# Performance work log

Measured on AMD Instinct MI355X. Metric: run time of the kernel, lower is better.

Reference implementation:

```python
import jax, jax.numpy as jnp
import numpy as np

R_FACTOR = 5  # reduction factor r from Tacotron.__init__


def _gru(x, h, Wx, Wh, b):
    # standard GRU cell: z,r,candidate gates packed along last dim of Wx/Wh/b
    H = h.shape[-1]
    gx = x @ Wx
    gh = h @ Wh
    z = jax.nn.sigmoid(gx[..., :H] + gh[..., :H] + b[:H])
    r = jax.nn.sigmoid(gx[..., H:2 * H] + gh[..., H:2 * H] + b[H:2 * H])
    c = jnp.tanh(gx[..., 2 * H:] + r * gh[..., 2 * H:] + b[2 * H:])
    return (1.0 - z) * h + z * c


def setup_inputs() -> dict:
    key = jax.random.key(0)
    ks = jax.random.split(key, 16)
    T_out, B, D = 1000, 128, 80     # decoder frames, batch, mel dim
    T_in, H, P = 512, 256, 128      # encoder steps, hidden, prenet out
    n = lambda k, shp, d: jax.random.normal(k, shp, dtype=jnp.float32) * (1.0 / np.sqrt(d))
    return {
        "outputs": jax.random.normal(ks[0], (T_out, B, D), dtype=jnp.float32),
        "memory": jax.random.normal(ks[1], (T_in, B, H), dtype=jnp.float32),
        "W_pre0": n(ks[2], (D, H), D), "b_pre0": jnp.zeros((H,), jnp.float32),
        "W_pre1": n(ks[3], (H, P), H), "b_pre1": jnp.zeros((P,), jnp.float32),
        "Wx_att": n(ks[4], (P, 3 * H), P), "Wh_att": n(ks[5], (H, 3 * H), H), "b_att": jnp.zeros((3 * H,), jnp.float32),
        "Wq": n(ks[6], (H, H), H), "Wm": n(ks[7], (H, H), H), "v_att": n(ks[8], (H,), H),
        "Wx_d0": n(ks[9], (2 * H, 3 * H), 2 * H), "Wh_d0": n(ks[10], (H, 3 * H), H), "b_d0": jnp.zeros((3 * H,), jnp.float32),
        "Wx_d1": n(ks[11], (H, 3 * H), H), "Wh_d1": n(ks[12], (H, 3 * H), H), "b_d1": jnp.zeros((3 * H,), jnp.float32),
        "Wo": n(ks[13], (H, D), H), "bo": jnp.zeros((D,), jnp.float32),
    }


def _forward(outputs, memory, W_pre0, b_pre0, W_pre1, b_pre1, Wx_att, Wh_att, b_att,
             Wq, Wm, v_att, Wx_d0, Wh_d0, b_d0, Wx_d1, Wh_d1, b_d1, Wo, bo):
    r = R_FACTOR
    T_out, B, D = outputs.shape
    H = memory.shape[-1]
    R = T_out // r  # reduced_time_steps
    # teacher-forcing frame per reduced step: indic[t*r + r - 1] with r zero-frames
    # prepended == outputs[t*r - 1] for t>=1, zeros for t=0.
    frames = jnp.concatenate(
        [jnp.zeros((1, B, D), outputs.dtype), outputs[r - 1::r][: R - 1]], axis=0)  # [R,B,D]
    # precompute attention keys once (AttModule over static memory)
    keys = jnp.einsum('tbh,hk->tbk', memory, Wm)  # [T_in,B,H]
    h0 = jnp.zeros((B, H), outputs.dtype)

    def step(state, frame):
        h_att, h_d0, h_d1 = state
        # pre-net (dropout inactive: inference-mode reference)
        pre = jax.nn.relu(frame @ W_pre0 + b_pre0)
        pre = jax.nn.relu(pre @ W_pre1 + b_pre1)
        # attention RNN
        query = _gru(pre, h_att, Wx_att, Wh_att, b_att)  # [B,H]
        # additive attention
        e = jnp.einsum('tbk,k->tb', jnp.tanh(keys + query @ Wq), v_att)  # [T_in,B]
        alpha = jax.nn.softmax(e, axis=0)
        context = jnp.einsum('tb,tbh->bh', alpha, memory)  # [B,H]
        # decoder cell 0 conditioned on context, with residual from query
        out0 = _gru(jnp.concatenate([query, context], axis=-1), h_d0, Wx_d0, Wh_d0, b_d0)
        res0 = query + out0
        # residual-wrapped decoder cell 1
        out1 = _gru(res0, h_d1, Wx_d1, Wh_d1, b_d1)
        res1 = res0 + out1
        dense = res1 @ Wo + bo  # [B,D]
        return (query, out0, out1), (dense, alpha)

    _, (dense_seq, alpha_seq) = jax.lax.scan(step, (h0, h0, h0), frames)
    # each reduced-step output is written to r consecutive output frames
    final_output = jnp.repeat(dense_seq, r, axis=0)  # [T_out,B,D]
    return final_output, alpha_seq  # alpha_seq: [R,B,T_in]... axes (R,T_in,B) -> transpose


def reference(outputs, memory, W_pre0, b_pre0, W_pre1, b_pre1, Wx_att, Wh_att, b_att,
              Wq, Wm, v_att, Wx_d0, Wh_d0, b_d0, Wx_d1, Wh_d1, b_d1, Wo, bo):
    final_output, alpha_seq = _forward(outputs, memory, W_pre0, b_pre0, W_pre1, b_pre1,
                                       Wx_att, Wh_att, b_att, Wq, Wm, v_att,
                                       Wx_d0, Wh_d0, b_d0, Wx_d1, Wh_d1, b_d1, Wo, bo)
    # alpha stacked per reduced step, shape [R, T_in, B] -> [R, B, T_in] as in TF reshape
    final_alpha = jnp.transpose(alpha_seq, (0, 2, 1))
    return final_output, final_alpha
```

## Files before the change

### kernel.cpp

```cpp
#include <hip/hip_runtime.h>

namespace {
constexpr int B = 128;
constexpr int D = 80;
constexpr int H = 256;
constexpr int PP = 128;
constexpr int TIN = 512;
constexpr int RSTEPS = 200;
constexpr int RF = 5;
constexpr int HB = H * B;
}

__device__ __forceinline__ float sigm(float x) { return 1.f / (1.f + __expf(-x)); }
__device__ __forceinline__ float tanh_(float x) { return 1.f - 2.f / (__expf(2.f * x) + 1.f); }
__device__ __forceinline__ unsigned short f2bf(float f) {
  unsigned int u = __float_as_uint(f);
  u += 0x7fffu + ((u >> 16) & 1u);
  return (unsigned short)(u >> 16);
}
__device__ __forceinline__ void bf2x(unsigned int w, float& f0, float& f1) {
  f0 = __uint_as_float(w << 16);
  f1 = __uint_as_float(w & 0xffff0000u);
}
__device__ __forceinline__ void unpack8(uint4 w, float* f) {
  bf2x(w.x, f[0], f[1]); bf2x(w.y, f[2], f[3]);
  bf2x(w.z, f[4], f[5]); bf2x(w.w, f[6], f[7]);
}
__device__ __forceinline__ float dot8(uint4 w, float4 x0, float4 x1) {
  float f0, f1, a;
  bf2x(w.x, f0, f1); a  = f0 * x0.x + f1 * x0.y;
  bf2x(w.y, f0, f1); a += f0 * x0.z + f1 * x0.w;
  bf2x(w.z, f0, f1); a += f0 * x1.x + f1 * x1.y;
  bf2x(w.w, f0, f1); a += f0 * x1.z + f1 * x1.w;
  return a;
}

__global__ __launch_bounds__(256) void k_keys(const float* __restrict__ mem,
                                              const float* __restrict__ Wm,
                                              unsigned short* __restrict__ keysB,
                                              unsigned short* __restrict__ memB) {
  const int k = threadIdx.x;
  const int bb = blockIdx.x >> 4, t0 = (blockIdx.x & 15) * 32;
  const float* base = mem + (size_t)t0 * (B * H) + (size_t)bb * H;
  float acc[32];
#pragma unroll
  for (int i = 0; i < 32; ++i) acc[i] = 0.f;
  for (int h = 0; h < H; h += 4) {
    const float w0 = Wm[(h + 0) * H + k];
    const float w1 = Wm[(h + 1) * H + k];
    const float w2 = Wm[(h + 2) * H + k];
    const float w3 = Wm[(h + 3) * H + k];
#pragma unroll
    for (int ti = 0; ti < 32; ++ti) {
      const float4 x = *reinterpret_cast<const float4*>(base + (size_t)ti * (B * H) + h);
      acc[ti] += x.x * w0 + x.y * w1 + x.z * w2 + x.w * w3;
    }
  }
#pragma unroll
  for (int ti = 0; ti < 32; ++ti) {
    const size_t o = ((size_t)bb * TIN + t0 + ti) * H + k;
    keysB[o] = f2bf(acc[ti]);
    memB[o] = f2bf(base[(size_t)ti * (B * H) + k]);
  }
}

__global__ __launch_bounds__(256) void k_packWq(const float* __restrict__ W,
                                                unsigned short* __restrict__ Wp) {
  const int idx = blockIdx.x * 256 + threadIdx.x;
  const int k = idx >> 8, c = idx & 255;
  Wp[(((size_t)(k >> 3) * 256) + c) * 8 + (k & 7)] = f2bf(W[idx]);
}

__global__ __launch_bounds__(256) void k_packG(const float* __restrict__ W,
                                               unsigned short* __restrict__ dst,
                                               int K, int rowOff) {
  const int idx = blockIdx.x * 256 + threadIdx.x;
  if (idx >= K * 768) return;
  const int k = idx / 768, c = idx - k * 768;
  const int g = c >> 8, j = c & 255;
  dst[((size_t)(rowOff + k) * 128 + (j >> 1)) * 8 + (j & 1) * 4 + g] = f2bf(W[idx]);
}

__global__ __launch_bounds__(256) void k_prenet(
    const float* __restrict__ outs, const float* __restrict__ Wp0,
    const float* __restrict__ bp0, const float* __restrict__ Wp1,
    const float* __restrict__ bp1, float* __restrict__ preT) {
  const int t = blockIdx.x >> 7, b = blockIdx.x & 127, tid = threadIdx.x;
  __shared__ float f[80];
  __shared__ float p0[256];
  __shared__ float s2[256];
  if (tid < 80)
    f[tid] = (t == 0) ? 0.f
                      : __builtin_nontemporal_load(
                            &outs[((size_t)(t * RF - 1) * B + b) * D + tid]);
  __syncthreads();
  {
    float a = bp0[tid];
#pragma unroll 8
    for (int k = 0; k < 80; ++k) a += f[k] * Wp0[k * 256 + tid];
    p0[tid] = fmaxf(a, 0.f);
  }
  __syncthreads();
  {
    const int c = tid & 127, kh = tid >> 7;
    float a = 0.f;
#pragma unroll 8
    for (int k = kh * 128; k < kh * 128 + 128; ++k) a += p0[k] * Wp1[k * 128 + c];
    s2[kh * 128 + c] = a;
  }
  __syncthreads();
  if (tid < 128)
    preT[((size_t)t * PP + tid) * B + b] = fmaxf(bp1[tid] + s2[tid] + s2[128 + tid], 0.f);
}

template <int NJP>
__device__ void gru_body(const unsigned short* __restrict__ wp, int K1, int K2,
                         int KH, const float* __restrict__ xT1,
                         const float* __restrict__ xT2,
                         const float* __restrict__ pctx0,
                         const float* __restrict__ msp,
                         const float* __restrict__ hT_old,
                         const float* __restrict__ b3, float* __restrict__ hT_new,
                         const float* __restrict__ resInT,
                         float* __restrict__ resOutT, int rel, float* smem) {
  const int tid = threadIdx.x;
  float* part = smem;
  float* red = smem + 8 * NJP * 512;
  const int grp = rel >> 1, bh = rel & 1;
  const int lane = tid & 63, wv = tid >> 6;
  const int b = bh * 64 + lane;

  float c0 = 0.f, c1 = 0.f;
  if (pctx0) {
    const float m0 = msp[b], s0 = msp[B + b];
    const float m1 = msp[2 * B + b], s1 = msp[3 * B + b];
    const float M = fmaxf(m0, m1);
    const float e0 = __expf(m0 - M), e1 = __expf(m1 - M);
    const float inv = 1.f / (s0 * e0 + s1 * e1);
    c0 = e0 * inv; c1 = e1 * inv;
  }

  const uint4* wp4 = reinterpret_cast<const uint4*>(wp);
  const int K12 = K1 + K2, KT = K12 + KH;
  const int KS = KT >> 3;
  const int k0 = wv * KS, k1 = k0 + KS;

  float acc[NJP * 8];
#pragma unroll
  for (int i = 0; i < NJP * 8; ++i) acc[i] = 0.f;
  float f0, f1;

#define UPD(wq, xv, base, CS)                                                  \
  bf2x(wq.x, f0, f1); acc[base + 0] += f0 * xv; acc[base + 1] += f1 * xv;      \
  bf2x(wq.y, f0, f1); acc[base + CS] += f0 * xv;                               \
  bf2x(wq.z, f0, f1); acc[base + 4] += f0 * xv; acc[base + 5] += f1 * xv;      \
  bf2x(wq.w, f0, f1); acc[base + 4 + CS] += f0 * xv;

  const int e1i = (k1 < K1) ? k1 : K1;
#pragma unroll 2
  for (int k = k0; k < e1i; ++k) {
    const float x = xT1[k * B + b];
#pragma unroll
    for (int p = 0; p < NJP; ++p) {
      const uint4 w = wp4[(size_t)k * 128 + grp * NJP + p];
      UPD(w, x, p * 8, 2)
    }
  }
  const int s2i = (k0 > K1) ? k0 : K1, e2i = (k1 < K12) ? k1 : K12;
#pragma unroll 2
  for (int k = s2i; k < e2i; ++k) {
    const int kk = k - K1;
    const float x = pctx0 ? (c0 * pctx0[kk * B + b] + c1 * pctx0[(256 + kk) * B + b])
                          : xT2[kk * B + b];
#pragma unroll
    for (int p = 0; p < NJP; ++p) {
      const uint4 w = wp4[(size_t)k * 128 + grp * NJP + p];
      UPD(w, x, p * 8, 2)
    }
  }
  const int s3i = (k0 > K12) ? k0 : K12;
#pragma unroll 2
  for (int k = s3i; k < k1; ++k) {
    const float x = hT_old[(k - K12) * B + b];
#pragma unroll
    for (int p = 0; p < NJP; ++p) {
      const uint4 w = wp4[(size_t)k * 128 + grp * NJP + p];
      UPD(w, x, p * 8, 3)
    }
  }
#undef UPD

  float* pw = part + wv * (NJP * 512);
#pragma unroll
  for (int i = 0; i < NJP * 8; ++i) pw[i * 64 + lane] = acc[i];
  __syncthreads();
  for (int idx = tid; idx < NJP * 512; idx += 512) {
    float s = 0.f;
#pragma unroll
    for (int w = 0; w < 8; ++w) s += part[w * (NJP * 512) + idx];
    red[idx] = s;
  }
  __syncthreads();
  if (tid < NJP * 128) {
    const int jl = tid >> 6, ln = tid & 63;
    const int j = grp * (NJP * 2) + jl;
    const int bb = bh * 64 + ln;
    const float az = red[(jl * 4 + 0) * 64 + ln];
    const float ar = red[(jl * 4 + 1) * 64 + ln];
    const float acx = red[(jl * 4 + 2) * 64 + ln];
    const float ach = red[(jl * 4 + 3) * 64 + ln];
    const float z = sigm(az + b3[j]);
    const float r = sigm(ar + b3[H + j]);
    const float c = tanh_(acx + r * ach + b3[2 * H + j]);
    const float hold = hT_old[j * B + bb];
    const float hn = (1.f - z) * hold + z * c;
    hT_new[j * B + bb] = hn;
    if (resOutT) resOutT[j * B + bb] = resInT[j * B + bb] + hn;
  }
}

__device__ void dense_body(int s, int b, const float* __restrict__ res1T,
                           const float* __restrict__ Wo,
                           const float* __restrict__ bo, float* __restrict__ dout,
                           const float* __restrict__ pvalsS,
                           const float* __restrict__ msS,
                           float* __restrict__ alpha, float* smem) {
  const int tid = threadIdx.x;
  float* red = smem;
  float* part = smem + 256;
  if (tid < 256) red[tid] = res1T[tid * B + b];
  __syncthreads();
  {
    const int ks = tid >> 7, c = tid & 127;
    float a = 0.f;
    if (c < D) {
#pragma unroll 8
      for (int k = ks * 64; k < ks * 64 + 64; ++k) a += red[k] * Wo[k * D + c];
    }
    part[ks * 128 + c] = a;
  }
  __syncthreads();
  if (tid < D) {
    float dv = bo[tid];
#pragma unroll
    for (int ks = 0; ks < 4; ++ks) dv += part[ks * 128 + tid];
    const size_t base = (size_t)s * RF * (B * D) + (size_t)b * D + tid;
#pragma unroll
    for (int i = 0; i < RF; ++i)
      __builtin_nontemporal_store(dv, &dout[base + (size_t)i * (B * D)]);
  }
  const float m0 = msS[b], s0 = msS[B + b], m1 = msS[2 * B + b], s1 = msS[3 * B + b];
  const float M = fmaxf(m0, m1);
  const float f0 = __expf(m0 - M), f1 = __expf(m1 - M);
  const float inv = 1.f / (s0 * f0 + s1 * f1);
  const float cc = (tid < 256) ? f0 * inv : f1 * inv;
  __builtin_nontemporal_store(pvalsS[(size_t)b * TIN + tid] * cc,
                              &alpha[((size_t)s * B + b) * TIN + tid]);
}

__device__ void attn_half_body(int b, int half, const float* __restrict__ qT,
                               const unsigned short* __restrict__ wqB,
                               const float* __restrict__ v_att,
                               const unsigned short* __restrict__ keysB,
                               const unsigned short* __restrict__ memB,
                               float* __restrict__ pvalsS, float* __restrict__ pctxS,
                               float* __restrict__ msS, float* smem) {
  const int tid = threadIdx.x;
  const int lane = tid & 63, wv = tid >> 6;
  const int t0 = half * 256;
  float* hA = smem;
  float* qk_p = smem + 256;
  float* v_p = smem + 544;
  float* scr = smem + 832;
  float* ep = smem + 4928;
  float* r16 = smem + 5184;
  float* bc = smem + 5200;

  if (tid < 256) {
    hA[tid] = qT[tid * B + b];
    v_p[(tid >> 4) * 18 + (tid & 15)] = v_att[tid];
  }
  __syncthreads();
  const float4* hA4 = reinterpret_cast<const float4*>(hA);
  const uint4* wQ = reinterpret_cast<const uint4*>(wqB);

  {
    const int c = tid & 255, ks = tid >> 8;
    float a = 0.f;
#pragma unroll
    for (int q = 0; q < 16; ++q) {
      const int kg = ks * 16 + q;
      a += dot8(wQ[(size_t)kg * 256 + c], hA4[kg * 2], hA4[kg * 2 + 1]);
    }
    scr[ks * 256 + c] = a;
  }
  __syncthreads();
  if (tid < 256)
    qk_p[(tid >> 4) * 18 + (tid & 15)] = scr[tid] + scr[256 + tid];
  __syncthreads();

  {
    const int l16 = tid & 15, g = tid >> 4;
    float qg[16], vg[16];
#pragma unroll
    for (int i = 0; i < 16; ++i) {
      qg[i] = qk_p[l16 * 18 + i];
      vg[i] = v_p[l16 * 18 + i];
    }
    const uint4* kB = reinterpret_cast<const uint4*>(keysB + (size_t)b * TIN * H);
#pragma unroll
    for (int p = 0; p < 4; ++p) {
      const int r1 = g + p * 64, r2 = r1 + 32;
      const uint4 a0 = kB[(size_t)(t0 + r1) * 32 + l16 * 2];
      const uint4 a1 = kB[(size_t)(t0 + r1) * 32 + l16 * 2 + 1];
      const uint4 b0 = kB[(size_t)(t0 + r2) * 32 + l16 * 2];
      const uint4 b1 = kB[(size_t)(t0 + r2) * 32 + l16 * 2 + 1];
      float ka[16], kb2[16];
      unpack8(a0, ka); unpack8(a1, ka + 8);
      unpack8(b0, kb2); unpack8(b1, kb2 + 8);
      float s1 = 0.f, s2 = 0.f;
#pragma unroll
      for (int i = 0; i < 16; ++i) {
        s1 += vg[i] * tanh_(ka[i] + qg[i]);
        s2 += vg[i] * tanh_(kb2[i] + qg[i]);
      }
#pragma unroll
      for (int m = 1; m < 16; m <<= 1) { s1 += __shfl_xor(s1, m, 16); s2 += __shfl_xor(s2, m, 16); }
      if (l16 == 0) { ep[r1] = s1; ep[r2] = s2; }
    }
  }
  __syncthreads();

  float ev = -1e30f, pv = 0.f;
  if (tid < 256) {
    ev = ep[tid];
    float mx = ev;
#pragma unroll
    for (int m = 1; m < 64; m <<= 1) mx = fmaxf(mx, __shfl_xor(mx, m));
    if (lane == 0) r16[wv] = mx;
  }
  __syncthreads();
  if (tid == 0)
    bc[0] = fmaxf(fmaxf(r16[0], r16[1]), fmaxf(r16[2], r16[3]));
  __syncthreads();
  const float M = bc[0];
  if (tid < 256) {
    pv = __expf(ev - M);
    ep[tid] = pv;
    pvalsS[(size_t)b * TIN + t0 + tid] = pv;
    float s = pv;
#pragma unroll
    for (int m = 1; m < 64; m <<= 1) s += __shfl_xor(s, m);
    if (lane == 0) r16[wv] = s;
  }
  __syncthreads();
  if (tid == 0) {
    msS[half * 2 * B + b] = M;
    msS[(half * 2 + 1) * B + b] = r16[0] + r16[1] + r16[2] + r16[3];
  }

  {
    const int kq8 = tid & 31, ts = tid >> 5;
    float a[8] = {0.f, 0.f, 0.f, 0.f, 0.f, 0.f, 0.f, 0.f};
    const uint4* mB = reinterpret_cast<const uint4*>(memB + (size_t)b * TIN * H);
#pragma unroll 4
    for (int i = 0; i < 16; ++i) {
      const int tt = ts * 16 + i;
      const float p = ep[tt];
      float mv[8];
      unpack8(mB[(size_t)(t0 + tt) * 32 + kq8], mv);
#pragma unroll
      for (int j = 0; j < 8; ++j) a[j] += p * mv[j];
    }
    float4* s4 = reinterpret_cast<float4*>(scr + ts * 256 + kq8 * 8);
    s4[0] = make_float4(a[0], a[1], a[2], a[3]);
    s4[1] = make_float4(a[4], a[5], a[6], a[7]);
  }
  __syncthreads();
  if (tid < 256) {
    float s = 0.f;
#pragma unroll
    for (int ts2 = 0; ts2 < 16; ++ts2) s += scr[ts2 * 256 + tid];
    pctxS[(size_t)(half * 256 + tid) * B + b] = s;
  }
}

__global__ __launch_bounds__(512, 8) void k_pipe(
    int i, const unsigned short* __restrict__ wgA,
    const unsigned short* __restrict__ wg0, const unsigned short* __restrict__ wg1,
    const unsigned short* __restrict__ wqB, const float* __restrict__ v_att,
    const float* __restrict__ b_att, const float* __restrict__ b_d0,
    const float* __restrict__ b_d1, const unsigned short* __restrict__ keysB,
    const unsigned short* __restrict__ memB, const float* __restrict__ preT,
    float* __restrict__ qr, float* __restrict__ hd0r, float* __restrict__ hd1r,
    float* __restrict__ res0r, float* __restrict__ res1r,
    float* __restrict__ pvals, float* __restrict__ pctx, float* __restrict__ ms,
    const float* __restrict__ Wo, const float* __restrict__ bo,
    float* __restrict__ dout, float* __restrict__ alpha) {
  __shared__ alignas(16) float smem[9216];
  const int blk = blockIdx.x;
  if (blk < 256) {
    const int t = i - 1;
    if (t >= 0 && t < RSTEPS) {
      const int sl = t & 3;
      attn_half_body(blk >> 1, blk & 1, qr + (size_t)sl * HB, wqB, v_att, keysB,
                     memB, pvals + (size_t)sl * B * TIN,
                     pctx + (size_t)sl * 2 * HB, ms + (size_t)sl * 4 * B, smem);
    }
  } else if (blk < 512) {
    const int t = i - 2;
    if (t >= 0 && t < RSTEPS) {
      const int sl = t & 3;
      gru_body<1>(wg0, H, H, H, qr + (size_t)sl * HB, nullptr,
                  pctx + (size_t)sl * 2 * HB, ms + (size_t)sl * 4 * B,
                  hd0r + (size_t)((t + 3) & 3) * HB, b_d0,
                  hd0r + (size_t)sl * HB, qr + (size_t)sl * HB,
                  res0r + (size_t)sl * HB, blk - 256, smem);
    }
  } else if (blk < 768) {
    const int t = i;
    if (t < RSTEPS)
      gru_body<1>(wgA, PP, 0, H, preT + (size_t)t * PP * B, nullptr, nullptr,
                  nullptr, qr + (size_t)((t + 3) & 3) * HB, b_att,
                  qr + (size_t)(t & 3) * HB, nullptr, nullptr, blk - 512, smem);
  } else if (blk < 896) {
    const int t = i - 3;
    if (t >= 0 && t < RSTEPS) {
      const int sl = t & 3;
      gru_body<2>(wg1, H, 0, H, res0r + (size_t)sl * HB, nullptr, nullptr,
                  nullptr, hd1r + (size_t)((t + 3) & 3) * HB, b_d1,
                  hd1r + (size_t)sl * HB, res0r + (size_t)sl * HB,
                  res1r + (size_t)sl * HB, blk - 768, smem);
    }
  } else {
    const int t = i - 4;
    if (t >= 0 && t < RSTEPS) {
      const int sl = t & 3;
      dense_body(t, blk - 896, res1r + (size_t)sl * HB, Wo, bo, dout,
                 pvals + (size_t)sl * B * TIN, ms + (size_t)sl * 4 * B, alpha,
                 smem);
    }
  }
}

extern "C" void kernel_launch(void* const* d_in, const int* in_sizes, int n_in,
                              void* d_out, int out_size, void* d_ws,
                              size_t ws_size, hipStream_t stream) {
  const float* outs   = (const float*)d_in[0];
  const float* memory = (const float*)d_in[1];
  const float* Wp0    = (const float*)d_in[2];
  const float* bp0    = (const float*)d_in[3];
  const float* Wp1    = (const float*)d_in[4];
  const float* bp1    = (const float*)d_in[5];
  const float* Wx_att = (const float*)d_in[6];
  const float* Wh_att = (const float*)d_in[7];
  const float* b_att  = (const float*)d_in[8];
  const float* Wq     = (const float*)d_in[9];
  const float* Wm     = (const float*)d_in[10];
  const float* v_att  = (const float*)d_in[11];
  const float* Wx_d0  = (const float*)d_in[12];
  const float* Wh_d0  = (const float*)d_in[13];
  const float* b_d0   = (const float*)d_in[14];
  const float* Wx_d1  = (const float*)d_in[15];
  const float* Wh_d1  = (const float*)d_in[16];
  const float* b_d1   = (const float*)d_in[17];
  const float* Wo     = (const float*)d_in[18];
  const float* bo     = (const float*)d_in[19];
  float* dout = (float*)d_out;
  float* wsf  = (float*)d_ws;

  size_t off = 0;
  unsigned short* keysB = (unsigned short*)(wsf + off); off += (size_t)TIN * B * H / 2;
  unsigned short* memB  = (unsigned short*)(wsf + off); off += (size_t)TIN * B * H / 2;
  unsigned short* wqB   = (unsigned short*)(wsf + off); off += (size_t)256 * 256 / 2;
  unsigned short* wgA   = (unsigned short*)(wsf + off); off += (size_t)384 * 1024 / 2;
  unsigned short* wg0   = (unsigned short*)(wsf + off); off += (size_t)768 * 1024 / 2;
  unsigned short* wg1   = (unsigned short*)(wsf + off); off += (size_t)512 * 1024 / 2;
  float* preT  = wsf + off; off += (size_t)RSTEPS * PP * B;
  float* qr    = wsf + off; off += (size_t)4 * HB;
  float* hd0r  = wsf + off; off += (size_t)4 * HB;
  float* hd1r  = wsf + off; off += (size_t)4 * HB;
  float* res0r = wsf + off; off += (size_t)4 * HB;
  float* res1r = wsf + off; off += (size_t)4 * HB;
  float* pvals = wsf + off; off += (size_t)4 * B * TIN;
  float* pctx  = wsf + off; off += (size_t)4 * 2 * HB;
  float* ms    = wsf + off; off += (size_t)4 * 4 * B;

  hipMemsetAsync(qr + 3 * HB, 0, (size_t)HB * sizeof(float), stream);
  hipMemsetAsync(hd0r + 3 * HB, 0, (size_t)HB * sizeof(float), stream);
  hipMemsetAsync(hd1r + 3 * HB, 0, (size_t)HB * sizeof(float), stream);

  k_keys<<<B * 16, 256, 0, stream>>>(memory, Wm, keysB, memB);
  k_prenet<<<RSTEPS * B, 256, 0, stream>>>(outs, Wp0, bp0, Wp1, bp1, preT);
  k_packWq<<<256, 256, 0, stream>>>(Wq, wqB);
  k_packG<<<(128 * 768 + 255) / 256, 256, 0, stream>>>(Wx_att, wgA, 128, 0);
  k_packG<<<(256 * 768 + 255) / 256, 256, 0, stream>>>(Wh_att, wgA, 256, 128);
  k_packG<<<(512 * 768 + 255) / 256, 256, 0, stream>>>(Wx_d0, wg0, 512, 0);
  k_packG<<<(256 * 768 + 255) / 256, 256, 0, stream>>>(Wh_d0, wg0, 256, 512);
  k_packG<<<(256 * 768 + 255) / 256, 256, 0, stream>>>(Wx_d1, wg1, 256, 0);
  k_packG<<<(256 * 768 + 255) / 256, 256, 0, stream>>>(Wh_d1, wg1, 256, 256);

  float* alpha = dout + (size_t)1000 * B * D;

  for (int i = 0; i < RSTEPS + 4; ++i) {
    k_pipe<<<1024, 512, 0, stream>>>(i, wgA, wg0, wg1, wqB, v_att, b_att,
                                     b_d0, b_d1, keysB, memB, preT, qr, hd0r,
                                     hd1r, res0r, res1r, pvals, pctx, ms, Wo,
                                     bo, dout, alpha);
  }
}
```

Baseline: 7.502 ms.

## Split attention into quarters, rebalance GRU block counts, restructure keys precompute

```diff
diff --git a/kernel.cpp b/kernel.cpp
--- a/kernel.cpp
+++ b/kernel.cpp
@@ -37,11 +37,10 @@
 
 __global__ __launch_bounds__(256) void k_keys(const float* __restrict__ mem,
                                               const float* __restrict__ Wm,
-                                              unsigned short* __restrict__ keysB,
-                                              unsigned short* __restrict__ memB) {
+                                              unsigned short* __restrict__ keysB) {
   const int k = threadIdx.x;
-  const int bb = blockIdx.x >> 4, t0 = (blockIdx.x & 15) * 32;
-  const float* base = mem + (size_t)t0 * (B * H) + (size_t)bb * H;
+  const int m0 = blockIdx.x * 32;
+  const float* xb = mem + (size_t)m0 * H;
   float acc[32];
 #pragma unroll
   for (int i = 0; i < 32; ++i) acc[i] = 0.f;
@@ -51,17 +50,22 @@
     const float w2 = Wm[(h + 2) * H + k];
     const float w3 = Wm[(h + 3) * H + k];
 #pragma unroll
-    for (int ti = 0; ti < 32; ++ti) {
-      const float4 x = *reinterpret_cast<const float4*>(base + (size_t)ti * (B * H) + h);
-      acc[ti] += x.x * w0 + x.y * w1 + x.z * w2 + x.w * w3;
-    }
-  }
-#pragma unroll
-  for (int ti = 0; ti < 32; ++ti) {
-    const size_t o = ((size_t)bb * TIN + t0 + ti) * H + k;
-    keysB[o] = f2bf(acc[ti]);
-    memB[o] = f2bf(base[(size_t)ti * (B * H) + k]);
-  }
+    for (int mi = 0; mi < 32; ++mi) {
+      const float4 x = *reinterpret_cast<const float4*>(xb + (size_t)mi * H + h);
+      acc[mi] += x.x * w0 + x.y * w1 + x.z * w2 + x.w * w3;
+    }
+  }
+#pragma unroll
+  for (int mi = 0; mi < 32; ++mi) {
+    const int m = m0 + mi, t = m >> 7, bb = m & 127;
+    keysB[((size_t)bb * TIN + t) * H + k] = f2bf(acc[mi]);
+  }
+}
+
+__global__ __launch_bounds__(256) void k_memB(const float* __restrict__ mem,
+                                              unsigned short* __restrict__ memB) {
+  const int m = blockIdx.x, t = m >> 7, bb = m & 127;
+  memB[((size_t)bb * TIN + t) * H + threadIdx.x] = f2bf(mem[(size_t)m * H + threadIdx.x]);
 }
 
 __global__ __launch_bounds__(256) void k_packWq(const float* __restrict__ W,
@@ -130,14 +134,17 @@
   const int lane = tid & 63, wv = tid >> 6;
   const int b = bh * 64 + lane;
 
-  float c0 = 0.f, c1 = 0.f;
+  float cq0 = 0.f, cq1 = 0.f, cq2 = 0.f, cq3 = 0.f;
   if (pctx0) {
     const float m0 = msp[b], s0 = msp[B + b];
     const float m1 = msp[2 * B + b], s1 = msp[3 * B + b];
-    const float M = fmaxf(m0, m1);
+    const float m2 = msp[4 * B + b], s2 = msp[5 * B + b];
+    const float m3 = msp[6 * B + b], s3 = msp[7 * B + b];
+    const float M = fmaxf(fmaxf(m0, m1), fmaxf(m2, m3));
     const float e0 = __expf(m0 - M), e1 = __expf(m1 - M);
-    const float inv = 1.f / (s0 * e0 + s1 * e1);
-    c0 = e0 * inv; c1 = e1 * inv;
+    const float e2 = __expf(m2 - M), e3 = __expf(m3 - M);
+    const float inv = 1.f / (s0 * e0 + s1 * e1 + s2 * e2 + s3 * e3);
+    cq0 = e0 * inv; cq1 = e1 * inv; cq2 = e2 * inv; cq3 = e3 * inv;
   }
 
   const uint4* wp4 = reinterpret_cast<const uint4*>(wp);
@@ -170,7 +177,8 @@
 #pragma unroll 2
   for (int k = s2i; k < e2i; ++k) {
     const int kk = k - K1;
-    const float x = pctx0 ? (c0 * pctx0[kk * B + b] + c1 * pctx0[(256 + kk) * B + b])
+    const float x = pctx0 ? (cq0 * pctx0[kk * B + b] + cq1 * pctx0[(256 + kk) * B + b] +
+                             cq2 * pctx0[(512 + kk) * B + b] + cq3 * pctx0[(768 + kk) * B + b])
                           : xT2[kk * B + b];
 #pragma unroll
     for (int p = 0; p < NJP; ++p) {
@@ -249,32 +257,37 @@
     for (int i = 0; i < RF; ++i)
       __builtin_nontemporal_store(dv, &dout[base + (size_t)i * (B * D)]);
   }
-  const float m0 = msS[b], s0 = msS[B + b], m1 = msS[2 * B + b], s1 = msS[3 * B + b];
-  const float M = fmaxf(m0, m1);
-  const float f0 = __expf(m0 - M), f1 = __expf(m1 - M);
-  const float inv = 1.f / (s0 * f0 + s1 * f1);
-  const float cc = (tid < 256) ? f0 * inv : f1 * inv;
+  const float m0 = msS[b], s0 = msS[B + b];
+  const float m1 = msS[2 * B + b], s1 = msS[3 * B + b];
+  const float m2 = msS[4 * B + b], s2 = msS[5 * B + b];
+  const float m3 = msS[6 * B + b], s3 = msS[7 * B + b];
+  const float M = fmaxf(fmaxf(m0, m1), fmaxf(m2, m3));
+  const float e0 = __expf(m0 - M), e1 = __expf(m1 - M);
+  const float e2 = __expf(m2 - M), e3 = __expf(m3 - M);
+  const float inv = 1.f / (s0 * e0 + s1 * e1 + s2 * e2 + s3 * e3);
+  const int q = tid >> 7;
+  const float cc = ((q == 0) ? e0 : (q == 1) ? e1 : (q == 2) ? e2 : e3) * inv;
   __builtin_nontemporal_store(pvalsS[(size_t)b * TIN + tid] * cc,
                               &alpha[((size_t)s * B + b) * TIN + tid]);
 }
 
-__device__ void attn_half_body(int b, int half, const float* __restrict__ qT,
-                               const unsigned short* __restrict__ wqB,
-                               const float* __restrict__ v_att,
-                               const unsigned short* __restrict__ keysB,
-                               const unsigned short* __restrict__ memB,
-                               float* __restrict__ pvalsS, float* __restrict__ pctxS,
-                               float* __restrict__ msS, float* smem) {
+__device__ void attn_q_body(int b, int quarter, const float* __restrict__ qT,
+                            const unsigned short* __restrict__ wqB,
+                            const float* __restrict__ v_att,
+                            const unsigned short* __restrict__ keysB,
+                            const unsigned short* __restrict__ memB,
+                            float* __restrict__ pvalsS, float* __restrict__ pctxS,
+                            float* __restrict__ msS, float* smem) {
   const int tid = threadIdx.x;
   const int lane = tid & 63, wv = tid >> 6;
-  const int t0 = half * 256;
+  const int t0 = quarter * 128;
   float* hA = smem;
   float* qk_p = smem + 256;
   float* v_p = smem + 544;
   float* scr = smem + 832;
   float* ep = smem + 4928;
-  float* r16 = smem + 5184;
-  float* bc = smem + 5200;
+  float* r16 = smem + 5056;
+  float* bc = smem + 5072;
 
   if (tid < 256) {
     hA[tid] = qT[tid * B + b];
@@ -309,7 +322,7 @@
     }
     const uint4* kB = reinterpret_cast<const uint4*>(keysB + (size_t)b * TIN * H);
 #pragma unroll
-    for (int p = 0; p < 4; ++p) {
+    for (int p = 0; p < 2; ++p) {
       const int r1 = g + p * 64, r2 = r1 + 32;
       const uint4 a0 = kB[(size_t)(t0 + r1) * 32 + l16 * 2];
       const uint4 a1 = kB[(size_t)(t0 + r1) * 32 + l16 * 2 + 1];
@@ -332,7 +345,7 @@
   __syncthreads();
 
   float ev = -1e30f, pv = 0.f;
-  if (tid < 256) {
+  if (tid < 128) {
     ev = ep[tid];
     float mx = ev;
 #pragma unroll
@@ -340,11 +353,10 @@
     if (lane == 0) r16[wv] = mx;
   }
   __syncthreads();
-  if (tid == 0)
-    bc[0] = fmaxf(fmaxf(r16[0], r16[1]), fmaxf(r16[2], r16[3]));
+  if (tid == 0) bc[0] = fmaxf(r16[0], r16[1]);
   __syncthreads();
   const float M = bc[0];
-  if (tid < 256) {
+  if (tid < 128) {
     pv = __expf(ev - M);
     ep[tid] = pv;
     pvalsS[(size_t)b * TIN + t0 + tid] = pv;
@@ -355,8 +367,8 @@
   }
   __syncthreads();
   if (tid == 0) {
-    msS[half * 2 * B + b] = M;
-    msS[(half * 2 + 1) * B + b] = r16[0] + r16[1] + r16[2] + r16[3];
+    msS[quarter * 2 * B + b] = M;
+    msS[(quarter * 2 + 1) * B + b] = r16[0] + r16[1];
   }
 
   {
@@ -364,8 +376,8 @@
     float a[8] = {0.f, 0.f, 0.f, 0.f, 0.f, 0.f, 0.f, 0.f};
     const uint4* mB = reinterpret_cast<const uint4*>(memB + (size_t)b * TIN * H);
 #pragma unroll 4
-    for (int i = 0; i < 16; ++i) {
-      const int tt = ts * 16 + i;
+    for (int i = 0; i < 8; ++i) {
+      const int tt = ts * 8 + i;
       const float p = ep[tt];
       float mv[8];
       unpack8(mB[(size_t)(t0 + tt) * 32 + kq8], mv);
@@ -381,7 +393,7 @@
     float s = 0.f;
 #pragma unroll
     for (int ts2 = 0; ts2 < 16; ++ts2) s += scr[ts2 * 256 + tid];
-    pctxS[(size_t)(half * 256 + tid) * B + b] = s;
+    pctxS[(size_t)(quarter * 256 + tid) * B + b] = s;
   }
 }
 
@@ -399,30 +411,30 @@
     float* __restrict__ dout, float* __restrict__ alpha) {
   __shared__ alignas(16) float smem[9216];
   const int blk = blockIdx.x;
-  if (blk < 256) {
+  if (blk < 512) {
     const int t = i - 1;
     if (t >= 0 && t < RSTEPS) {
       const int sl = t & 3;
-      attn_half_body(blk >> 1, blk & 1, qr + (size_t)sl * HB, wqB, v_att, keysB,
-                     memB, pvals + (size_t)sl * B * TIN,
-                     pctx + (size_t)sl * 2 * HB, ms + (size_t)sl * 4 * B, smem);
-    }
-  } else if (blk < 512) {
+      attn_q_body(blk >> 2, blk & 3, qr + (size_t)sl * HB, wqB, v_att, keysB,
+                  memB, pvals + (size_t)sl * B * TIN,
+                  pctx + (size_t)sl * 4 * HB, ms + (size_t)sl * 8 * B, smem);
+    }
+  } else if (blk < 640) {
+    const int t = i;
+    if (t < RSTEPS)
+      gru_body<2>(wgA, PP, 0, H, preT + (size_t)t * PP * B, nullptr, nullptr,
+                  nullptr, qr + (size_t)((t + 3) & 3) * HB, b_att,
+                  qr + (size_t)(t & 3) * HB, nullptr, nullptr, blk - 512, smem);
+  } else if (blk < 768) {
     const int t = i - 2;
     if (t >= 0 && t < RSTEPS) {
       const int sl = t & 3;
-      gru_body<1>(wg0, H, H, H, qr + (size_t)sl * HB, nullptr,
-                  pctx + (size_t)sl * 2 * HB, ms + (size_t)sl * 4 * B,
+      gru_body<2>(wg0, H, H, H, qr + (size_t)sl * HB, nullptr,
+                  pctx + (size_t)sl * 4 * HB, ms + (size_t)sl * 8 * B,
                   hd0r + (size_t)((t + 3) & 3) * HB, b_d0,
                   hd0r + (size_t)sl * HB, qr + (size_t)sl * HB,
-                  res0r + (size_t)sl * HB, blk - 256, smem);
-    }
-  } else if (blk < 768) {
-    const int t = i;
-    if (t < RSTEPS)
-      gru_body<1>(wgA, PP, 0, H, preT + (size_t)t * PP * B, nullptr, nullptr,
-                  nullptr, qr + (size_t)((t + 3) & 3) * HB, b_att,
-                  qr + (size_t)(t & 3) * HB, nullptr, nullptr, blk - 512, smem);
+                  res0r + (size_t)sl * HB, blk - 640, smem);
+    }
   } else if (blk < 896) {
     const int t = i - 3;
     if (t >= 0 && t < RSTEPS) {
@@ -437,7 +449,7 @@
     if (t >= 0 && t < RSTEPS) {
       const int sl = t & 3;
       dense_body(t, blk - 896, res1r + (size_t)sl * HB, Wo, bo, dout,
-                 pvals + (size_t)sl * B * TIN, ms + (size_t)sl * 4 * B, alpha,
+                 pvals + (size_t)sl * B * TIN, ms + (size_t)sl * 8 * B, alpha,
                  smem);
     }
   }
@@ -483,14 +495,15 @@
   float* res0r = wsf + off; off += (size_t)4 * HB;
   float* res1r = wsf + off; off += (size_t)4 * HB;
   float* pvals = wsf + off; off += (size_t)4 * B * TIN;
-  float* pctx  = wsf + off; off += (size_t)4 * 2 * HB;
-  float* ms    = wsf + off; off += (size_t)4 * 4 * B;
+  float* pctx  = wsf + off; off += (size_t)4 * 4 * HB;
+  float* ms    = wsf + off; off += (size_t)4 * 8 * B;
 
   hipMemsetAsync(qr + 3 * HB, 0, (size_t)HB * sizeof(float), stream);
   hipMemsetAsync(hd0r + 3 * HB, 0, (size_t)HB * sizeof(float), stream);
   hipMemsetAsync(hd1r + 3 * HB, 0, (size_t)HB * sizeof(float), stream);
 
-  k_keys<<<B * 16, 256, 0, stream>>>(memory, Wm, keysB, memB);
+  k_keys<<<(TIN * B) / 32, 256, 0, stream>>>(memory, Wm, keysB);
+  k_memB<<<TIN * B, 256, 0, stream>>>(memory, memB);
   k_prenet<<<RSTEPS * B, 256, 0, stream>>>(outs, Wp0, bp0, Wp1, bp1, preT);
   k_packWq<<<256, 256, 0, stream>>>(Wq, wqB);
   k_packG<<<(128 * 768 + 255) / 256, 256, 0, stream>>>(Wx_att, wgA, 128, 0);
```

Result: slower. 9.099 ms (+21.3%).

## Split query projection into its own pipeline stage and rebalance GRU block counts

Applied to the files above, without the earlier changes.

```diff
diff --git a/kernel.cpp b/kernel.cpp
--- a/kernel.cpp
+++ b/kernel.cpp
@@ -37,11 +37,10 @@
 
 __global__ __launch_bounds__(256) void k_keys(const float* __restrict__ mem,
                                               const float* __restrict__ Wm,
-                                              unsigned short* __restrict__ keysB,
-                                              unsigned short* __restrict__ memB) {
+                                              unsigned short* __restrict__ keysB) {
   const int k = threadIdx.x;
-  const int bb = blockIdx.x >> 4, t0 = (blockIdx.x & 15) * 32;
-  const float* base = mem + (size_t)t0 * (B * H) + (size_t)bb * H;
+  const int m0 = blockIdx.x * 32;
+  const float* xb = mem + (size_t)m0 * H;
   float acc[32];
 #pragma unroll
   for (int i = 0; i < 32; ++i) acc[i] = 0.f;
@@ -51,17 +50,22 @@
     const float w2 = Wm[(h + 2) * H + k];
     const float w3 = Wm[(h + 3) * H + k];
 #pragma unroll
-    for (int ti = 0; ti < 32; ++ti) {
-      const float4 x = *reinterpret_cast<const float4*>(base + (size_t)ti * (B * H) + h);
-      acc[ti] += x.x * w0 + x.y * w1 + x.z * w2 + x.w * w3;
-    }
-  }
-#pragma unroll
-  for (int ti = 0; ti < 32; ++ti) {
-    const size_t o = ((size_t)bb * TIN + t0 + ti) * H + k;
-    keysB[o] = f2bf(acc[ti]);
-    memB[o] = f2bf(base[(size_t)ti * (B * H) + k]);
-  }
+    for (int mi = 0; mi < 32; ++mi) {
+      const float4 x = *reinterpret_cast<const float4*>(xb + (size_t)mi * H + h);
+      acc[mi] += x.x * w0 + x.y * w1 + x.z * w2 + x.w * w3;
+    }
+  }
+#pragma unroll
+  for (int mi = 0; mi < 32; ++mi) {
+    const int m = m0 + mi, t = m >> 7, bb = m & 127;
+    keysB[((size_t)bb * TIN + t) * H + k] = f2bf(acc[mi]);
+  }
+}
+
+__global__ __launch_bounds__(256) void k_memB(const float* __restrict__ mem,
+                                              unsigned short* __restrict__ memB) {
+  const int m = blockIdx.x, t = m >> 7, bb = m & 127;
+  memB[((size_t)bb * TIN + t) * H + threadIdx.x] = f2bf(mem[(size_t)m * H + threadIdx.x]);
 }
 
 __global__ __launch_bounds__(256) void k_packWq(const float* __restrict__ W,
@@ -219,6 +223,28 @@
   }
 }
 
+__device__ void qw_body(int b, const float* __restrict__ qT,
+                        const unsigned short* __restrict__ wqB,
+                        float* __restrict__ qkT, float* smem) {
+  const int tid = threadIdx.x;
+  float* hA = smem;
+  float* scr = smem + 256;
+  if (tid < 256) hA[tid] = qT[tid * B + b];
+  __syncthreads();
+  const float4* hA4 = reinterpret_cast<const float4*>(hA);
+  const uint4* wQ = reinterpret_cast<const uint4*>(wqB);
+  const int c = tid & 255, ks = tid >> 8;
+  float a = 0.f;
+#pragma unroll
+  for (int q = 0; q < 16; ++q) {
+    const int kg = ks * 16 + q;
+    a += dot8(wQ[(size_t)kg * 256 + c], hA4[kg * 2], hA4[kg * 2 + 1]);
+  }
+  scr[ks * 256 + c] = a;
+  __syncthreads();
+  if (tid < 256) qkT[tid * B + b] = scr[tid] + scr[256 + tid];
+}
+
 __device__ void dense_body(int s, int b, const float* __restrict__ res1T,
                            const float* __restrict__ Wo,
                            const float* __restrict__ bo, float* __restrict__ dout,
@@ -258,8 +284,7 @@
                               &alpha[((size_t)s * B + b) * TIN + tid]);
 }
 
-__device__ void attn_half_body(int b, int half, const float* __restrict__ qT,
-                               const unsigned short* __restrict__ wqB,
+__device__ void attn_half_body(int b, int half, const float* __restrict__ qkT,
                                const float* __restrict__ v_att,
                                const unsigned short* __restrict__ keysB,
                                const unsigned short* __restrict__ memB,
@@ -268,35 +293,17 @@
   const int tid = threadIdx.x;
   const int lane = tid & 63, wv = tid >> 6;
   const int t0 = half * 256;
-  float* hA = smem;
-  float* qk_p = smem + 256;
-  float* v_p = smem + 544;
-  float* scr = smem + 832;
-  float* ep = smem + 4928;
-  float* r16 = smem + 5184;
-  float* bc = smem + 5200;
+  float* qk_p = smem;
+  float* v_p = smem + 288;
+  float* scr = smem + 576;
+  float* ep = smem + 4672;
+  float* r16 = smem + 4928;
+  float* bc = smem + 4944;
 
   if (tid < 256) {
-    hA[tid] = qT[tid * B + b];
+    qk_p[(tid >> 4) * 18 + (tid & 15)] = qkT[tid * B + b];
     v_p[(tid >> 4) * 18 + (tid & 15)] = v_att[tid];
   }
-  __syncthreads();
-  const float4* hA4 = reinterpret_cast<const float4*>(hA);
-  const uint4* wQ = reinterpret_cast<const uint4*>(wqB);
-
-  {
-    const int c = tid & 255, ks = tid >> 8;
-    float a = 0.f;
-#pragma unroll
-    for (int q = 0; q < 16; ++q) {
-      const int kg = ks * 16 + q;
-      a += dot8(wQ[(size_t)kg * 256 + c], hA4[kg * 2], hA4[kg * 2 + 1]);
-    }
-    scr[ks * 256 + c] = a;
-  }
-  __syncthreads();
-  if (tid < 256)
-    qk_p[(tid >> 4) * 18 + (tid & 15)] = scr[tid] + scr[256 + tid];
   __syncthreads();
 
   {
@@ -392,51 +399,58 @@
     const float* __restrict__ b_att, const float* __restrict__ b_d0,
     const float* __restrict__ b_d1, const unsigned short* __restrict__ keysB,
     const unsigned short* __restrict__ memB, const float* __restrict__ preT,
-    float* __restrict__ qr, float* __restrict__ hd0r, float* __restrict__ hd1r,
-    float* __restrict__ res0r, float* __restrict__ res1r,
+    float* __restrict__ qr, float* __restrict__ qkr, float* __restrict__ hd0r,
+    float* __restrict__ hd1r, float* __restrict__ res0r, float* __restrict__ res1r,
     float* __restrict__ pvals, float* __restrict__ pctx, float* __restrict__ ms,
     const float* __restrict__ Wo, const float* __restrict__ bo,
     float* __restrict__ dout, float* __restrict__ alpha) {
   __shared__ alignas(16) float smem[9216];
   const int blk = blockIdx.x;
   if (blk < 256) {
+    const int t = i - 2;
+    if (t >= 0 && t < RSTEPS) {
+      const int sl = t & 3;
+      attn_half_body(blk >> 1, blk & 1, qkr + (size_t)sl * (256 * B), v_att,
+                     keysB, memB, pvals + (size_t)sl * B * TIN,
+                     pctx + (size_t)sl * 2 * HB, ms + (size_t)sl * 4 * B, smem);
+    }
+  } else if (blk < 384) {
+    const int t = i;
+    if (t < RSTEPS)
+      gru_body<2>(wgA, PP, 0, H, preT + (size_t)t * PP * B, nullptr, nullptr,
+                  nullptr, qr + (size_t)((t + 3) & 3) * HB, b_att,
+                  qr + (size_t)(t & 3) * HB, nullptr, nullptr, blk - 256, smem);
+  } else if (blk < 512) {
     const int t = i - 1;
     if (t >= 0 && t < RSTEPS) {
       const int sl = t & 3;
-      attn_half_body(blk >> 1, blk & 1, qr + (size_t)sl * HB, wqB, v_att, keysB,
-                     memB, pvals + (size_t)sl * B * TIN,
-                     pctx + (size_t)sl * 2 * HB, ms + (size_t)sl * 4 * B, smem);
-    }
-  } else if (blk < 512) {
-    const int t = i - 2;
+      qw_body(blk - 384, qr + (size_t)sl * HB, wqB,
+              qkr + (size_t)sl * (256 * B), smem);
+    }
+  } else if (blk < 640) {
+    const int t = i - 3;
     if (t >= 0 && t < RSTEPS) {
       const int sl = t & 3;
-      gru_body<1>(wg0, H, H, H, qr + (size_t)sl * HB, nullptr,
+      gru_body<2>(wg0, H, H, H, qr + (size_t)sl * HB, nullptr,
                   pctx + (size_t)sl * 2 * HB, ms + (size_t)sl * 4 * B,
                   hd0r + (size_t)((t + 3) & 3) * HB, b_d0,
                   hd0r + (size_t)sl * HB, qr + (size_t)sl * HB,
-                  res0r + (size_t)sl * HB, blk - 256, smem);
+                  res0r + (size_t)sl * HB, blk - 512, smem);
     }
   } else if (blk < 768) {
-    const int t = i;
-    if (t < RSTEPS)
-      gru_body<1>(wgA, PP, 0, H, preT + (size_t)t * PP * B, nullptr, nullptr,
-                  nullptr, qr + (size_t)((t + 3) & 3) * HB, b_att,
-                  qr + (size_t)(t & 3) * HB, nullptr, nullptr, blk - 512, smem);
-  } else if (blk < 896) {
-    const int t = i - 3;
+    const int t = i - 4;
     if (t >= 0 && t < RSTEPS) {
       const int sl = t & 3;
       gru_body<2>(wg1, H, 0, H, res0r + (size_t)sl * HB, nullptr, nullptr,
                   nullptr, hd1r + (size_t)((t + 3) & 3) * HB, b_d1,
                   hd1r + (size_t)sl * HB, res0r + (size_t)sl * HB,
-                  res1r + (size_t)sl * HB, blk - 768, smem);
+                  res1r + (size_t)sl * HB, blk - 640, smem);
     }
   } else {
-    const int t = i - 4;
+    const int t = i - 5;
     if (t >= 0 && t < RSTEPS) {
       const int sl = t & 3;
-      dense_body(t, blk - 896, res1r + (size_t)sl * HB, Wo, bo, dout,
+      dense_body(t, blk - 768, res1r + (size_t)sl * HB, Wo, bo, dout,
                  pvals + (size_t)sl * B * TIN, ms + (size_t)sl * 4 * B, alpha,
                  smem);
     }
@@ -478,6 +492,7 @@
   unsigned short* wg1   = (unsigned short*)(wsf + off); off += (size_t)512 * 1024 / 2;
   float* preT  = wsf + off; off += (size_t)RSTEPS * PP * B;
   float* qr    = wsf + off; off += (size_t)4 * HB;
+  float* qkr   = wsf + off; off += (size_t)4 * 256 * B;
   float* hd0r  = wsf + off; off += (size_t)4 * HB;
   float* hd1r  = wsf + off; off += (size_t)4 * HB;
   float* res0r = wsf + off; off += (size_t)4 * HB;
@@ -490,7 +505,8 @@
   hipMemsetAsync(hd0r + 3 * HB, 0, (size_t)HB * sizeof(float), stream);
   hipMemsetAsync(hd1r + 3 * HB, 0, (size_t)HB * sizeof(float), stream);
 
-  k_keys<<<B * 16, 256, 0, stream>>>(memory, Wm, keysB, memB);
+  k_keys<<<(TIN * B) / 32, 256, 0, stream>>>(memory, Wm, keysB);
+  k_memB<<<TIN * B, 256, 0, stream>>>(memory, memB);
   k_prenet<<<RSTEPS * B, 256, 0, stream>>>(outs, Wp0, bp0, Wp1, bp1, preT);
   k_packWq<<<256, 256, 0, stream>>>(Wq, wqB);
   k_packG<<<(128 * 768 + 255) / 256, 256, 0, stream>>>(Wx_att, wgA, 128, 0);
@@ -502,10 +518,10 @@
 
   float* alpha = dout + (size_t)1000 * B * D;
 
-  for (int i = 0; i < RSTEPS + 4; ++i) {
-    k_pipe<<<1024, 512, 0, stream>>>(i, wgA, wg0, wg1, wqB, v_att, b_att,
-                                     b_d0, b_d1, keysB, memB, preT, qr, hd0r,
-                                     hd1r, res0r, res1r, pvals, pctx, ms, Wo,
-                                     bo, dout, alpha);
-  }
-}
+  for (int i = 0; i < RSTEPS + 5; ++i) {
+    k_pipe<<<896, 512, 0, stream>>>(i, wgA, wg0, wg1, wqB, v_att, b_att,
+                                    b_d0, b_d1, keysB, memB, preT, qr, qkr,
+                                    hd0r, hd1r, res0r, res1r, pvals, pctx, ms,
+                                    Wo, bo, dout, alpha);
+  }
+}
```

Result: slower. 9.434 ms (+25.8%).
